# Performance work log

Measured on AMD Instinct MI355X. Metric: run time of the kernel, lower is better.

Reference implementation:

```python
import jax, jax.numpy as jnp
import numpy as np

N_NODES = 100000
N_GRAPHS = 128
DIM = 64


def gcn_conv(x, edge_index, W, b, n_nodes):
    # PyG GCNConv: add self-loops, symmetric normalization D^-1/2 (A+I) D^-1/2,
    # linear transform (no bias in lin), then aggregate, then add bias.
    src, dst = edge_index[0], edge_index[1]
    loop = jnp.arange(n_nodes, dtype=src.dtype)
    src = jnp.concatenate([src, loop])
    dst = jnp.concatenate([dst, loop])
    deg = jax.ops.segment_sum(jnp.ones_like(src, dtype=x.dtype), dst,
                              num_segments=n_nodes)  # in-degree incl. self-loop
    dinv = jnp.where(deg > 0, jax.lax.rsqrt(deg), 0.0)
    norm = dinv[src] * dinv[dst]                      # [E+N]
    xw = x @ W                                        # [N, out]
    msg = xw[src] * norm[:, None]                     # gather + scale per edge
    out = jax.ops.segment_sum(msg, dst, num_segments=n_nodes)  # scatter-add
    return out + b


def global_mean_pool(x, batch, n_graphs):
    sums = jax.ops.segment_sum(x, batch, num_segments=n_graphs)
    cnt = jax.ops.segment_sum(jnp.ones((x.shape[0],), x.dtype), batch,
                              num_segments=n_graphs)
    return sums / jnp.maximum(cnt, 1.0)[:, None]


def setup_inputs() -> dict:
    key = jax.random.key(0)
    ks = jax.random.split(key, 12)
    scale = 1.0 / np.sqrt(DIM)
    x = jax.random.normal(ks[0], (N_NODES, DIM), dtype=jnp.float32)
    edge_index = jax.random.randint(ks[1], (2, 1600000), 0, N_NODES, dtype=jnp.int64)
    batch = jnp.sort(jax.random.randint(ks[2], (N_NODES,), 0, N_GRAPHS, dtype=jnp.int64))
    def w(k):
        return jax.random.uniform(k, (DIM, DIM), jnp.float32, -scale, scale)
    def b(k):
        return jax.random.uniform(k, (DIM,), jnp.float32, -scale, scale)
    return {
        "x": x, "edge_index": edge_index, "batch": batch,
        "W1": w(ks[3]), "b1": b(ks[4]),
        "W2": w(ks[5]), "b2": b(ks[6]),
        "W3": w(ks[7]), "b3": b(ks[8]),
        "Wlin": w(ks[9]), "blin": b(ks[10]),
    }


def reference(x, edge_index, batch, W1, b1, W2, b2, W3, b3, Wlin, blin):
    n = x.shape[0]
    h = jax.nn.relu(gcn_conv(x, edge_index, W1, b1, n))
    h = jax.nn.relu(gcn_conv(h, edge_index, W2, b2, n))
    h = gcn_conv(h, edge_index, W3, b3, n)
    g = global_mean_pool(h, batch, N_GRAPHS)   # [G, DIM]
    # dropout p=0.5 is identity in eval mode
    return g @ Wlin + blin
```

## Files before the change

### kernel.cpp

```cpp
#include <hip/hip_runtime.h>

#define DIM 64
#define NPW 8
#define NB_SHIFT 8
#define NB 256
#define BMAX 1024
#define TILE 4096
#define EPT 16


__global__ __launch_bounds__(256) void k_binA(const int* __restrict__ dst, int E, int B,
                                              int* __restrict__ bucketCnt) {
    __shared__ int cntL[BMAX];
    int t = threadIdx.x;
    for (int j = t; j < B; j += 256) cntL[j] = 0;
    __syncthreads();
    int stride = gridDim.x * 256;
    for (int i = blockIdx.x * 256 + t; i < E; i += stride)
        atomicAdd(&cntL[dst[i] >> NB_SHIFT], 1);
    __syncthreads();
    for (int j = t; j < B; j += 256)
        if (cntL[j]) atomicAdd(&bucketCnt[j], cntL[j]);
}

__global__ __launch_bounds__(256) void k_scanB(const int* __restrict__ bucketCnt, int B, int E, int N,
                                               int* __restrict__ bucketOff,
                                               int* __restrict__ bucketCursor,
                                               int* __restrict__ row_ptr) {
    __shared__ int sdata[256];
    int t = threadIdx.x;
    int i0 = 2 * t, i1 = 2 * t + 1;
    int a0 = (i0 < B) ? bucketCnt[i0] : 0;
    int a1 = (i1 < B) ? bucketCnt[i1] : 0;
    int s = a0 + a1;
    sdata[t] = s;
    __syncthreads();
    for (int off = 1; off < 256; off <<= 1) {
        int tmp = (t >= off) ? sdata[t - off] : 0;
        __syncthreads();
        if (t >= off) sdata[t] += tmp;
        __syncthreads();
    }
    int excl = sdata[t] - s;
    if (i0 <= B) { bucketOff[i0] = excl; if (i0 < B) bucketCursor[i0] = excl; }
    int o1 = excl + a0;
    if (i1 <= B) { bucketOff[i1] = o1; if (i1 < B) bucketCursor[i1] = o1; }
    if (t == 0) row_ptr[N] = E;
}

__global__ __launch_bounds__(256) void k_binB(const int* __restrict__ src, const int* __restrict__ dst,
                                              int E, int B, int* __restrict__ bucketCursor,
                                              int* __restrict__ pairs) {
    __shared__ int cntL[BMAX];
    __shared__ int baseL[BMAX];
    int t = threadIdx.x;
    for (int j = t; j < B; j += 256) cntL[j] = 0;
    __syncthreads();
    int tile0 = blockIdx.x * TILE;
    int s_[EPT], d_[EPT], o_[EPT];
#pragma unroll
    for (int j = 0; j < EPT; ++j) {
        int i = tile0 + j * 256 + t;
        if (i < E) {
            s_[j] = src[i];
            d_[j] = dst[i];
            o_[j] = atomicAdd(&cntL[d_[j] >> NB_SHIFT], 1);
        } else {
            d_[j] = -1;
        }
    }
    __syncthreads();
    for (int j = t; j < B; j += 256)
        if (cntL[j]) baseL[j] = atomicAdd(&bucketCursor[j], cntL[j]);
    __syncthreads();
#pragma unroll
    for (int j = 0; j < EPT; ++j) {
        if (d_[j] >= 0) {
            int b = d_[j] >> NB_SHIFT;
            pairs[baseL[b] + o_[j]] = ((d_[j] & (NB - 1)) << 17) | s_[j];
        }
    }
}

__global__ __launch_bounds__(256) void k_buildCSR(const int* __restrict__ pairs,
                                                  const int* __restrict__ bucketOff,
                                                  int N, int* __restrict__ row_ptr,
                                                  int* __restrict__ col,
                                                  float* __restrict__ dinv) {
    __shared__ int cntL[NB];
    __shared__ int sdata[NB];
    __shared__ int curL[NB];
    int t = threadIdx.x;
    int b = blockIdx.x;
    int nodeBase = b << NB_SHIFT;
    int nNodes = N - nodeBase; if (nNodes > NB) nNodes = NB;
    int e0 = bucketOff[b], e1 = bucketOff[b + 1];
    cntL[t] = 0;
    __syncthreads();
    for (int i = e0 + t; i < e1; i += 256)
        atomicAdd(&cntL[pairs[i] >> 17], 1);
    __syncthreads();
    int c = cntL[t];
    sdata[t] = c;
    __syncthreads();
    for (int off = 1; off < 256; off <<= 1) {
        int tmp = (t >= off) ? sdata[t - off] : 0;
        __syncthreads();
        if (t >= off) sdata[t] += tmp;
        __syncthreads();
    }
    int excl = sdata[t] - c;
    if (t < nNodes) {
        row_ptr[nodeBase + t] = e0 + excl;
        dinv[nodeBase + t] = rsqrtf((float)(c + 1));
    }
    curL[t] = excl;
    __syncthreads();
    for (int i = e0 + t; i < e1; i += 256) {
        int p = pairs[i];
        int l = p >> 17;
        int slot = atomicAdd(&curL[l], 1);
        col[e0 + slot] = p & 0x1FFFF;
    }
}

__global__ __launch_bounds__(256) void k_prep(const float* __restrict__ dinv, const float* __restrict__ x,
                                              int N, float* __restrict__ Xs) {
    int t = threadIdx.x;
    int lane = t & 63;
    int v = blockIdx.x * 4 + (t >> 6);
    if (v >= N) return;
    Xs[v * DIM + lane] = x[v * DIM + lane] * dinv[v];
}

template <bool RELU, bool SCALE_OUT>
__global__ __launch_bounds__(256, 8) void k_layer(const float* __restrict__ In,
                                                  const int* __restrict__ row_ptr,
                                                  const int* __restrict__ col,
                                                  const float* __restrict__ dinv,
                                                  const float* __restrict__ W,
                                                  const float* __restrict__ bias,
                                                  float* __restrict__ Out, int N) {
    __shared__ float WLs[DIM * DIM];
    __shared__ float4 zL[4 * 16];
    int t = threadIdx.x;
    int lane = t & 63;
    int wave = t >> 6;
    int g = lane >> 4;
    int gl = lane & 15;

    for (int k = wave; k < DIM; k += 4)
        WLs[(k >> 2) * 256 + lane * 4 + (k & 3)] = W[k * DIM + lane];
    __syncthreads();
    const float4* WL4 = (const float4*)WLs;

    float blane = bias[lane];
    const float4* InR = (const float4*)In;

    int v0 = (blockIdx.x * 4 + wave) * NPW;
    for (int r = 0; r < NPW; ++r) {
        int v = v0 + r;
        if (v >= N) return;
        int e0 = row_ptr[v];
        int e1 = row_ptr[v + 1];
        float dv = dinv[v];
        int d1 = e1 - e0 + 1;
        float4 acc0 = make_float4(0.f, 0.f, 0.f, 0.f);
        float4 acc1 = make_float4(0.f, 0.f, 0.f, 0.f);
        float4 acc2 = make_float4(0.f, 0.f, 0.f, 0.f);
        float4 acc3 = make_float4(0.f, 0.f, 0.f, 0.f);
        int base = 0;
        while (base < d1) {
            int m = d1 - base; if (m > 64) m = 64;
            int slot = base + lane;
            int u = v;
            if (slot > 0 && slot < d1) u = col[e0 + slot - 1];
            int nfull = m >> 2;
            int q = 0;
            for (; q + 4 <= nfull; q += 4) {
                int u0 = __shfl(u, (q + 0) * 4 + g, 64);
                int u1 = __shfl(u, (q + 1) * 4 + g, 64);
                int u2 = __shfl(u, (q + 2) * 4 + g, 64);
                int u3 = __shfl(u, (q + 3) * 4 + g, 64);
                float4 a0 = InR[u0 * 16 + gl];
                float4 a1 = InR[u1 * 16 + gl];
                float4 a2 = InR[u2 * 16 + gl];
                float4 a3 = InR[u3 * 16 + gl];
                acc0.x += a0.x; acc0.y += a0.y; acc0.z += a0.z; acc0.w += a0.w;
                acc1.x += a1.x; acc1.y += a1.y; acc1.z += a1.z; acc1.w += a1.w;
                acc2.x += a2.x; acc2.y += a2.y; acc2.z += a2.z; acc2.w += a2.w;
                acc3.x += a3.x; acc3.y += a3.y; acc3.z += a3.z; acc3.w += a3.w;
            }
            for (; q + 2 <= nfull; q += 2) {
                int u0 = __shfl(u, (q + 0) * 4 + g, 64);
                int u1 = __shfl(u, (q + 1) * 4 + g, 64);
                float4 a0 = InR[u0 * 16 + gl];
                float4 a1 = InR[u1 * 16 + gl];
                acc0.x += a0.x; acc0.y += a0.y; acc0.z += a0.z; acc0.w += a0.w;
                acc1.x += a1.x; acc1.y += a1.y; acc1.z += a1.z; acc1.w += a1.w;
            }
            for (; q < nfull; ++q) {
                int u0 = __shfl(u, q * 4 + g, 64);
                float4 a0 = InR[u0 * 16 + gl];
                acc0.x += a0.x; acc0.y += a0.y; acc0.z += a0.z; acc0.w += a0.w;
            }
            if (m & 3) {
                int sidx = nfull * 4 + g;
                bool ok = sidx < m;
                int uu = __shfl(u, ok ? sidx : 0, 64);
                float4 a0 = InR[uu * 16 + gl];
                if (ok) { acc0.x += a0.x; acc0.y += a0.y; acc0.z += a0.z; acc0.w += a0.w; }
            }
            base += m;
        }
        float4 z;
        z.x = (acc0.x + acc1.x) + (acc2.x + acc3.x);
        z.y = (acc0.y + acc1.y) + (acc2.y + acc3.y);
        z.z = (acc0.z + acc1.z) + (acc2.z + acc3.z);
        z.w = (acc0.w + acc1.w) + (acc2.w + acc3.w);
        z.x += __shfl_xor(z.x, 16, 64); z.y += __shfl_xor(z.y, 16, 64);
        z.z += __shfl_xor(z.z, 16, 64); z.w += __shfl_xor(z.w, 16, 64);
        z.x += __shfl_xor(z.x, 32, 64); z.y += __shfl_xor(z.y, 32, 64);
        z.z += __shfl_xor(z.z, 32, 64); z.w += __shfl_xor(z.w, 32, 64);
        if (g == 0) zL[wave * 16 + gl] = z;
        float rdot = 0.f;
#pragma unroll
        for (int k16 = 0; k16 < 16; ++k16) {
            float4 zc = zL[wave * 16 + k16];
            float4 wv = WL4[k16 * 64 + lane];
            rdot = fmaf(zc.x, wv.x, rdot);
            rdot = fmaf(zc.y, wv.y, rdot);
            rdot = fmaf(zc.z, wv.z, rdot);
            rdot = fmaf(zc.w, wv.w, rdot);
        }
        float h = fmaf(dv, rdot, blane);
        if (RELU) h = fmaxf(h, 0.f);
        if (SCALE_OUT) h *= dv;
        Out[v * DIM + lane] = h;
    }
}


__global__ __launch_bounds__(256) void k_pool(const float* __restrict__ H, const int* __restrict__ batch,
                                              int N, float* __restrict__ sums, int chunk) {
    int t = threadIdx.x;
    int lane = t & 63;
    int start = (blockIdx.x * 4 + (t >> 6)) * chunk;
    int end = start + chunk; if (end > N) end = N;
    if (start >= end) return;
    float acc = 0.f;
    int cur = batch[start];
    for (int i = start; i < end; ++i) {
        int b = batch[i];
        if (b != cur) {
            atomicAdd(&sums[cur * DIM + lane], acc);
            acc = 0.f; cur = b;
        }
        acc += H[i * DIM + lane];
    }
    atomicAdd(&sums[cur * DIM + lane], acc);
}

__global__ __launch_bounds__(64) void k_final(const float* __restrict__ sums,
                                              const int* __restrict__ batch, int N,
                                              const float* __restrict__ Wlin,
                                              const float* __restrict__ blin,
                                              float* __restrict__ out) {
    int g = blockIdx.x;
    int j = threadIdx.x;
    int lo = 0, hi = N;
    while (lo < hi) { int mid = (lo + hi) >> 1; if (batch[mid] < g) lo = mid + 1; else hi = mid; }
    int c0 = lo;
    lo = 0; hi = N;
    int g1 = g + 1;
    while (lo < hi) { int mid = (lo + hi) >> 1; if (batch[mid] < g1) lo = mid + 1; else hi = mid; }
    int c1 = lo;
    int c = c1 - c0; if (c < 1) c = 1;
    float invc = 1.0f / (float)c;
    float acc = 0.f;
#pragma unroll
    for (int k = 0; k < DIM; ++k)
        acc = fmaf(sums[g * DIM + k] * invc, Wlin[k * DIM + j], acc);
    out[g * DIM + j] = acc + blin[j];
}


extern "C" void kernel_launch(void* const* d_in, const int* in_sizes, int n_in,
                              void* d_out, int out_size, void* d_ws, size_t ws_size,
                              hipStream_t stream) {
    const float* x    = (const float*)d_in[0];
    const int*   edge = (const int*)d_in[1];
    const int*   batch= (const int*)d_in[2];
    const float* W1 = (const float*)d_in[3];
    const float* b1 = (const float*)d_in[4];
    const float* W2 = (const float*)d_in[5];
    const float* b2 = (const float*)d_in[6];
    const float* W3 = (const float*)d_in[7];
    const float* b3 = (const float*)d_in[8];
    const float* Wlin = (const float*)d_in[9];
    const float* blin = (const float*)d_in[10];
    float* out = (float*)d_out;

    int N = in_sizes[0] / DIM;
    int E = in_sizes[1] / 2;
    int G = out_size / DIM;
    const int* srcv = edge;
    const int* dstv = edge + E;
    int B = (N + NB - 1) >> NB_SHIFT;

    char* ws = (char*)d_ws;
    auto alloc = [&](size_t bytes) {
        char* p = ws;
        ws += (bytes + 255) & ~(size_t)255;
        return p;
    };
    int*   bucketCnt    = (int*)alloc((size_t)B * 4);
    int*   bucketOff    = (int*)alloc((size_t)(B + 1) * 4);
    int*   bucketCursor = (int*)alloc((size_t)B * 4);
    int*   pairs        = (int*)alloc((size_t)E * 4);
    int*   row_ptr      = (int*)alloc(((size_t)N + 1) * 4);
    int*   colv         = (int*)alloc((size_t)E * 4);
    float* dinv         = (float*)alloc((size_t)N * 4);
    float* Xs           = (float*)alloc((size_t)N * DIM * 4);
    float* buf0         = (float*)alloc((size_t)N * DIM * 4);
    float* buf1         = (float*)alloc((size_t)N * DIM * 4);
    float* sums         = (float*)alloc((size_t)G * DIM * 4);

    hipMemsetAsync(bucketCnt, 0, (size_t)B * 4, stream);
    hipMemsetAsync(sums, 0, (size_t)G * DIM * 4, stream);

    k_binA<<<512, 256, 0, stream>>>(dstv, E, B, bucketCnt);
    k_scanB<<<1, 256, 0, stream>>>(bucketCnt, B, E, N, bucketOff, bucketCursor, row_ptr);
    k_binB<<<(E + TILE - 1) / TILE, 256, 0, stream>>>(srcv, dstv, E, B, bucketCursor, pairs);
    k_buildCSR<<<B, 256, 0, stream>>>(pairs, bucketOff, N, row_ptr, colv, dinv);
    k_prep<<<(N + 3) / 4, 256, 0, stream>>>(dinv, x, N, Xs);

    int layerBlocks = (N + 4 * NPW - 1) / (4 * NPW);

    k_layer<true, true><<<layerBlocks, 256, 0, stream>>>(Xs, row_ptr, colv, dinv, W1, b1, buf0, N);
    k_layer<true, true><<<layerBlocks, 256, 0, stream>>>(buf0, row_ptr, colv, dinv, W2, b2, buf1, N);
    k_layer<false, false><<<layerBlocks, 256, 0, stream>>>(buf1, row_ptr, colv, dinv, W3, b3, buf0, N);

    int chunk = 64;
    int poolBlocks = (N + 4 * chunk - 1) / (4 * chunk);
    k_pool<<<poolBlocks, 256, 0, stream>>>(buf0, batch, N, sums, chunk);
    k_final<<<G, 64, 0, stream>>>(sums, batch, N, Wlin, blin, out);
}
```

Before: 392.5 us.

## Fuse prescale into CSR build and use register-resident W with shuffle reduction

Folds the x*dinv prescale into k_buildCSR, which removes the separate k_prep launch and the reread of dinv. In k_layer, each lane now keeps a 16-float4 slice of W in registers and computes the 64x64 matvec through a butterfly shuffle reduction, replacing the LDS round trip through zL. The extra registers force launch bounds to drop from 8 to 4 blocks per CU. NPW doubles to 16, which gives fewer, larger blocks and amortises the W load, at the cost of occupancy and load balance.

```diff
diff --git a/kernel.cpp b/kernel.cpp
--- a/kernel.cpp
+++ b/kernel.cpp
@@ -1,7 +1,7 @@
 #include <hip/hip_runtime.h>
 
 #define DIM 64
-#define NPW 8
+#define NPW 16
 #define NB_SHIFT 8
 #define NB 256
 #define BMAX 1024
@@ -86,10 +86,13 @@
                                                   const int* __restrict__ bucketOff,
                                                   int N, int* __restrict__ row_ptr,
                                                   int* __restrict__ col,
-                                                  float* __restrict__ dinv) {
+                                                  float* __restrict__ dinv,
+                                                  const float* __restrict__ x,
+                                                  float* __restrict__ Xs) {
     __shared__ int cntL[NB];
     __shared__ int sdata[NB];
     __shared__ int curL[NB];
+    __shared__ float dinvL[NB];
     int t = threadIdx.x;
     int b = blockIdx.x;
     int nodeBase = b << NB_SHIFT;
@@ -110,10 +113,12 @@
         __syncthreads();
     }
     int excl = sdata[t] - c;
+    float dv = rsqrtf((float)(c + 1));
     if (t < nNodes) {
         row_ptr[nodeBase + t] = e0 + excl;
-        dinv[nodeBase + t] = rsqrtf((float)(c + 1));
-    }
+        dinv[nodeBase + t] = dv;
+    }
+    dinvL[t] = dv;
     curL[t] = excl;
     __syncthreads();
     for (int i = e0 + t; i < e1; i += 256) {
@@ -122,19 +127,14 @@
         int slot = atomicAdd(&curL[l], 1);
         col[e0 + slot] = p & 0x1FFFF;
     }
-}
-
-__global__ __launch_bounds__(256) void k_prep(const float* __restrict__ dinv, const float* __restrict__ x,
-                                              int N, float* __restrict__ Xs) {
-    int t = threadIdx.x;
-    int lane = t & 63;
-    int v = blockIdx.x * 4 + (t >> 6);
-    if (v >= N) return;
-    Xs[v * DIM + lane] = x[v * DIM + lane] * dinv[v];
+    int total = nNodes * DIM;
+    int base64 = nodeBase << 6;
+    for (int i = t; i < total; i += 256)
+        Xs[base64 + i] = x[base64 + i] * dinvL[i >> 6];
 }
 
 template <bool RELU, bool SCALE_OUT>
-__global__ __launch_bounds__(256, 8) void k_layer(const float* __restrict__ In,
+__global__ __launch_bounds__(256, 4) void k_layer(const float* __restrict__ In,
                                                   const int* __restrict__ row_ptr,
                                                   const int* __restrict__ col,
                                                   const float* __restrict__ dinv,
@@ -142,7 +142,6 @@
                                                   const float* __restrict__ bias,
                                                   float* __restrict__ Out, int N) {
     __shared__ float WLs[DIM * DIM];
-    __shared__ float4 zL[4 * 16];
     int t = threadIdx.x;
     int lane = t & 63;
     int wave = t >> 6;
@@ -154,6 +153,12 @@
     __syncthreads();
     const float4* WL4 = (const float4*)WLs;
 
+    float4 wl[16];
+#pragma unroll
+    for (int s = 0; s < 16; ++s) {
+        int o = (lane & 48) | ((lane ^ s) & 15);
+        wl[s] = WL4[gl * 64 + o];
+    }
     float blane = bias[lane];
     const float4* InR = (const float4*)In;
 
@@ -222,18 +227,18 @@
         z.z += __shfl_xor(z.z, 16, 64); z.w += __shfl_xor(z.w, 16, 64);
         z.x += __shfl_xor(z.x, 32, 64); z.y += __shfl_xor(z.y, 32, 64);
         z.z += __shfl_xor(z.z, 32, 64); z.w += __shfl_xor(z.w, 32, 64);
-        if (g == 0) zL[wave * 16 + gl] = z;
-        float rdot = 0.f;
-#pragma unroll
-        for (int k16 = 0; k16 < 16; ++k16) {
-            float4 zc = zL[wave * 16 + k16];
-            float4 wv = WL4[k16 * 64 + lane];
-            rdot = fmaf(zc.x, wv.x, rdot);
-            rdot = fmaf(zc.y, wv.y, rdot);
-            rdot = fmaf(zc.z, wv.z, rdot);
-            rdot = fmaf(zc.w, wv.w, rdot);
-        }
-        float h = fmaf(dv, rdot, blane);
+        float q[16];
+#pragma unroll
+        for (int s = 0; s < 16; ++s)
+            q[s] = fmaf(z.x, wl[s].x, fmaf(z.y, wl[s].y, fmaf(z.z, wl[s].z, z.w * wl[s].w)));
+#pragma unroll
+        for (int d = 0; d < 8; ++d) q[d] += __shfl_xor(q[d ^ 8], 8, 64);
+#pragma unroll
+        for (int d = 0; d < 4; ++d) q[d] += __shfl_xor(q[d ^ 4], 4, 64);
+#pragma unroll
+        for (int d = 0; d < 2; ++d) q[d] += __shfl_xor(q[d ^ 2], 2, 64);
+        q[0] += __shfl_xor(q[1], 1, 64);
+        float h = fmaf(dv, q[0], blane);
         if (RELU) h = fmaxf(h, 0.f);
         if (SCALE_OUT) h *= dv;
         Out[v * DIM + lane] = h;
@@ -332,8 +337,7 @@
     k_binA<<<512, 256, 0, stream>>>(dstv, E, B, bucketCnt);
     k_scanB<<<1, 256, 0, stream>>>(bucketCnt, B, E, N, bucketOff, bucketCursor, row_ptr);
     k_binB<<<(E + TILE - 1) / TILE, 256, 0, stream>>>(srcv, dstv, E, B, bucketCursor, pairs);
-    k_buildCSR<<<B, 256, 0, stream>>>(pairs, bucketOff, N, row_ptr, colv, dinv);
-    k_prep<<<(N + 3) / 4, 256, 0, stream>>>(dinv, x, N, Xs);
+    k_buildCSR<<<B, 256, 0, stream>>>(pairs, bucketOff, N, row_ptr, colv, dinv, x, Xs);
 
     int layerBlocks = (N + 4 * NPW - 1) / (4 * NPW);
 
```

Result: slower. 443.8 us (+13.1%).

## Fuse x prescale into CSR build and merge pooling with output head

Applied to the files above, without the earlier changes.

The dinv-scaled copy of x is now produced inside the CSR build kernel from a shared-memory dinv array, which removes the separate prep kernel. Pooling and the final linear head are merged into one kernel with one block per graph. Each block finds its node range in the sorted batch array and sums rows directly, which removes the atomics, the sums buffer and its memset. The trade-off is that pooling now runs on only 128 blocks, so parallelism is lower, and the CSR build kernel carries extra streaming work.

```diff
diff --git a/kernel.cpp b/kernel.cpp
--- a/kernel.cpp
+++ b/kernel.cpp
@@ -86,10 +86,13 @@
                                                   const int* __restrict__ bucketOff,
                                                   int N, int* __restrict__ row_ptr,
                                                   int* __restrict__ col,
-                                                  float* __restrict__ dinv) {
+                                                  float* __restrict__ dinv,
+                                                  const float* __restrict__ x,
+                                                  float* __restrict__ Xs) {
     __shared__ int cntL[NB];
     __shared__ int sdata[NB];
     __shared__ int curL[NB];
+    __shared__ float dinvL[NB];
     int t = threadIdx.x;
     int b = blockIdx.x;
     int nodeBase = b << NB_SHIFT;
@@ -110,10 +113,12 @@
         __syncthreads();
     }
     int excl = sdata[t] - c;
+    float dv = rsqrtf((float)(c + 1));
     if (t < nNodes) {
         row_ptr[nodeBase + t] = e0 + excl;
-        dinv[nodeBase + t] = rsqrtf((float)(c + 1));
-    }
+        dinv[nodeBase + t] = dv;
+    }
+    dinvL[t] = dv;
     curL[t] = excl;
     __syncthreads();
     for (int i = e0 + t; i < e1; i += 256) {
@@ -122,15 +127,10 @@
         int slot = atomicAdd(&curL[l], 1);
         col[e0 + slot] = p & 0x1FFFF;
     }
-}
-
-__global__ __launch_bounds__(256) void k_prep(const float* __restrict__ dinv, const float* __restrict__ x,
-                                              int N, float* __restrict__ Xs) {
-    int t = threadIdx.x;
-    int lane = t & 63;
-    int v = blockIdx.x * 4 + (t >> 6);
-    if (v >= N) return;
-    Xs[v * DIM + lane] = x[v * DIM + lane] * dinv[v];
+    int total = nNodes * DIM;
+    int base64 = nodeBase << 6;
+    for (int i = t; i < total; i += 256)
+        Xs[base64 + i] = x[base64 + i] * dinvL[i >> 6];
 }
 
 template <bool RELU, bool SCALE_OUT>
@@ -240,48 +240,43 @@
     }
 }
 
-
-__global__ __launch_bounds__(256) void k_pool(const float* __restrict__ H, const int* __restrict__ batch,
-                                              int N, float* __restrict__ sums, int chunk) {
+__global__ __launch_bounds__(256) void k_poolhead(const float* __restrict__ H,
+                                                  const int* __restrict__ batch, int N,
+                                                  const float* __restrict__ Wlin,
+                                                  const float* __restrict__ blin,
+                                                  float* __restrict__ out) {
+    __shared__ float partial[4 * DIM];
+    __shared__ float meanL[DIM];
     int t = threadIdx.x;
     int lane = t & 63;
-    int start = (blockIdx.x * 4 + (t >> 6)) * chunk;
-    int end = start + chunk; if (end > N) end = N;
-    if (start >= end) return;
-    float acc = 0.f;
-    int cur = batch[start];
-    for (int i = start; i < end; ++i) {
-        int b = batch[i];
-        if (b != cur) {
-            atomicAdd(&sums[cur * DIM + lane], acc);
-            acc = 0.f; cur = b;
-        }
-        acc += H[i * DIM + lane];
-    }
-    atomicAdd(&sums[cur * DIM + lane], acc);
-}
-
-__global__ __launch_bounds__(64) void k_final(const float* __restrict__ sums,
-                                              const int* __restrict__ batch, int N,
-                                              const float* __restrict__ Wlin,
-                                              const float* __restrict__ blin,
-                                              float* __restrict__ out) {
-    int g = blockIdx.x;
-    int j = threadIdx.x;
+    int wave = t >> 6;
+    int gph = blockIdx.x;
     int lo = 0, hi = N;
-    while (lo < hi) { int mid = (lo + hi) >> 1; if (batch[mid] < g) lo = mid + 1; else hi = mid; }
+    while (lo < hi) { int mid = (lo + hi) >> 1; if (batch[mid] < gph) lo = mid + 1; else hi = mid; }
     int c0 = lo;
     lo = 0; hi = N;
-    int g1 = g + 1;
+    int g1 = gph + 1;
     while (lo < hi) { int mid = (lo + hi) >> 1; if (batch[mid] < g1) lo = mid + 1; else hi = mid; }
     int c1 = lo;
-    int c = c1 - c0; if (c < 1) c = 1;
-    float invc = 1.0f / (float)c;
     float acc = 0.f;
+    for (int i = c0 + wave; i < c1; i += 4)
+        acc += H[i * DIM + lane];
+    partial[wave * DIM + lane] = acc;
+    __syncthreads();
+    if (wave == 0) {
+        int c = c1 - c0; if (c < 1) c = 1;
+        float invc = 1.0f / (float)c;
+        float s = partial[lane] + partial[DIM + lane] + partial[2 * DIM + lane] + partial[3 * DIM + lane];
+        meanL[lane] = s * invc;
+    }
+    __syncthreads();
+    if (wave == 0) {
+        float r = blin[lane];
 #pragma unroll
-    for (int k = 0; k < DIM; ++k)
-        acc = fmaf(sums[g * DIM + k] * invc, Wlin[k * DIM + j], acc);
-    out[g * DIM + j] = acc + blin[j];
+        for (int k = 0; k < DIM; ++k)
+            r = fmaf(meanL[k], Wlin[k * DIM + lane], r);
+        out[gph * DIM + lane] = r;
+    }
 }
 
 
@@ -324,16 +319,13 @@
     float* Xs           = (float*)alloc((size_t)N * DIM * 4);
     float* buf0         = (float*)alloc((size_t)N * DIM * 4);
     float* buf1         = (float*)alloc((size_t)N * DIM * 4);
-    float* sums         = (float*)alloc((size_t)G * DIM * 4);
 
     hipMemsetAsync(bucketCnt, 0, (size_t)B * 4, stream);
-    hipMemsetAsync(sums, 0, (size_t)G * DIM * 4, stream);
 
     k_binA<<<512, 256, 0, stream>>>(dstv, E, B, bucketCnt);
     k_scanB<<<1, 256, 0, stream>>>(bucketCnt, B, E, N, bucketOff, bucketCursor, row_ptr);
     k_binB<<<(E + TILE - 1) / TILE, 256, 0, stream>>>(srcv, dstv, E, B, bucketCursor, pairs);
-    k_buildCSR<<<B, 256, 0, stream>>>(pairs, bucketOff, N, row_ptr, colv, dinv);
-    k_prep<<<(N + 3) / 4, 256, 0, stream>>>(dinv, x, N, Xs);
+    k_buildCSR<<<B, 256, 0, stream>>>(pairs, bucketOff, N, row_ptr, colv, dinv, x, Xs);
 
     int layerBlocks = (N + 4 * NPW - 1) / (4 * NPW);
 
@@ -341,8 +333,5 @@
     k_layer<true, true><<<layerBlocks, 256, 0, stream>>>(buf0, row_ptr, colv, dinv, W2, b2, buf1, N);
     k_layer<false, false><<<layerBlocks, 256, 0, stream>>>(buf1, row_ptr, colv, dinv, W3, b3, buf0, N);
 
-    int chunk = 64;
-    int poolBlocks = (N + 4 * chunk - 1) / (4 * chunk);
-    k_pool<<<poolBlocks, 256, 0, stream>>>(buf0, batch, N, sums, chunk);
-    k_final<<<G, 64, 0, stream>>>(sums, batch, N, Wlin, blin, out);
-}
+    k_poolhead<<<G, 256, 0, stream>>>(buf0, batch, N, Wlin, blin, out);
+}
```

Result: slower. 413.5 us (+5.4%).
